# Kernel optimization log

Measured on AMD Instinct MI355X. Metric: run time of the kernel, lower is better.

The kernel has to match this reference:

```python
import jax, jax.numpy as jnp
import numpy as np
import math

N_HEADS = 16
D_HEAD = 128
D_ROPE = 32
SPLIT = D_HEAD - D_ROPE  # 96
LATENT = 512
D_MODEL = 2048
B, T = 2, 2048


def _rotary_emb(num_tokens, d_rope):
    inv_freq = 1.0 / (10000.0 ** (jnp.arange(0, d_rope, 2, dtype=jnp.float32) / d_rope))
    t = jnp.arange(num_tokens, dtype=jnp.float32)
    freqs = jnp.einsum('t,f->tf', t, inv_freq)          # [T, d_rope/2]
    return jnp.concatenate([freqs, freqs], axis=-1)      # [T, d_rope]


def _apply_rotary(x, cos, sin):
    # x: [B,T,H,d_rope]; cos/sin: [1,T,1,d_rope]
    half = x.shape[-1] // 2
    x1, x2 = x[..., :half], x[..., half:]
    rot = jnp.concatenate([-x2, x1], axis=-1)
    return x * cos + rot * sin


def setup_inputs() -> dict:
    key = jax.random.key(0)
    ks = jax.random.split(key, 20)
    s = 0.02
    def w(k, i, o):
        return jax.random.normal(k, (i, o), dtype=jnp.float32) * s
    inp = {
        'input': jax.random.normal(ks[0], (B, T, D_MODEL), dtype=jnp.float32),
        'batch_size': B,
        'num_tokens': T,
        'Wdkv_w': w(ks[1], D_MODEL, LATENT), 'Wdkv_b': jnp.zeros((LATENT,), jnp.float32),
        'Wdq_w':  w(ks[2], D_MODEL, LATENT), 'Wdq_b':  jnp.zeros((LATENT,), jnp.float32),
        'Wuk_w':  w(ks[3], LATENT, N_HEADS * SPLIT),  'Wuk_b': jnp.zeros((N_HEADS * SPLIT,), jnp.float32),
        'Wuv_w':  w(ks[4], LATENT, N_HEADS * D_HEAD), 'Wuv_b': jnp.zeros((N_HEADS * D_HEAD,), jnp.float32),
        'Wuq_w':  w(ks[5], LATENT, N_HEADS * SPLIT),  'Wuq_b': jnp.zeros((N_HEADS * SPLIT,), jnp.float32),
        'Wqr_w':  w(ks[6], LATENT, N_HEADS * D_ROPE), 'Wqr_b': jnp.zeros((N_HEADS * D_ROPE,), jnp.float32),
        'Wkr_w':  w(ks[7], D_MODEL, N_HEADS * D_ROPE), 'Wkr_b': jnp.zeros((N_HEADS * D_ROPE,), jnp.float32),
        'Wo_w':   w(ks[8], N_HEADS * D_HEAD, D_MODEL), 'Wo_b': jnp.zeros((D_MODEL,), jnp.float32),
    }
    return inp


def reference(input, batch_size, num_tokens,
              Wdkv_w, Wdkv_b, Wdq_w, Wdq_b, Wuk_w, Wuk_b, Wuv_w, Wuv_b,
              Wuq_w, Wuq_b, Wqr_w, Wqr_b, Wkr_w, Wkr_b, Wo_w, Wo_b):
    lin = lambda x, w, b: x @ w + b
    bsz, T_ = batch_size, num_tokens

    c_kv = lin(input, Wdkv_w, Wdkv_b)                                   # [B,T,latent]
    k_base = lin(c_kv, Wuk_w, Wuk_b).reshape(bsz, T_, N_HEADS, SPLIT)
    v = lin(c_kv, Wuv_w, Wuv_b).reshape(bsz, T_, N_HEADS, D_HEAD)

    c_q = lin(input, Wdq_w, Wdq_b)
    q_base = lin(c_q, Wuq_w, Wuq_b).reshape(bsz, T_, N_HEADS, SPLIT)
    q_rot = lin(c_q, Wqr_w, Wqr_b).reshape(bsz, T_, N_HEADS, D_ROPE)

    emb = _rotary_emb(T_, D_ROPE)                                        # [T,d_rope]
    cos = jnp.cos(emb)[None, :, None, :]
    sin = jnp.sin(emb)[None, :, None, :]
    q_rot = _apply_rotary(q_rot, cos, sin)
    k_rot = _apply_rotary(lin(input, Wkr_w, Wkr_b).reshape(bsz, T_, N_HEADS, D_ROPE), cos, sin)

    q = jnp.concatenate([q_base, q_rot], axis=-1)                        # [B,T,H,d_head]
    k = jnp.concatenate([k_base, k_rot], axis=-1)

    scores = jnp.einsum('bqhd,bkhd->bhqk', q, k) / math.sqrt(D_HEAD)
    attn = jax.nn.softmax(scores, axis=-1)
    out = jnp.einsum('bhqk,bkhd->bqhd', attn, v)
    out = lin(out.reshape(bsz, T_, N_HEADS * D_HEAD), Wo_w, Wo_b)
    return out, c_kv, k_rot
```

## Files before the change

### kernel.cpp

```cpp
#include <hip/hip_runtime.h>

typedef __bf16 bf16x8 __attribute__((ext_vector_type(8)));
typedef float f32x4 __attribute__((ext_vector_type(4)));
typedef float f32x16 __attribute__((ext_vector_type(16)));

#define NROWS 4096
#define DM 2048
#define LAT 512
#define NH 16
#define DH 128

__device__ __forceinline__ unsigned short f2bf(float f) {
    union { float f; unsigned u; } v; v.f = f;
    unsigned r = v.u + 0x7fffu + ((v.u >> 16) & 1u);
    return (unsigned short)(r >> 16);
}
__device__ __forceinline__ void gload16(const void* g, void* l) {
    __builtin_amdgcn_global_load_lds((const __attribute__((address_space(1))) unsigned int*)g,
                                     (__attribute__((address_space(3))) unsigned int*)l, 16, 0, 0);
}
__device__ __forceinline__ unsigned cvtpk_bf16(float lo, float hi) {
    unsigned r;
    asm("v_cvt_pk_bf16_f32 %0, %1, %2" : "=v"(r) : "v"(lo), "v"(hi));
    return r;
}
__device__ __forceinline__ void pl32swap(unsigned& a, unsigned& b) {
    asm("v_permlane32_swap_b32 %0, %1" : "+v"(a), "+v"(b));
}
__device__ __forceinline__ float exp2a(float x) {
    float r;
    asm("v_exp_f32 %0, %1" : "=v"(r) : "v"(x));
    return r;
}

struct PrepParams {
    const float* tsrc[8]; unsigned short* tdst[8];
    int tK[8]; int tN[8]; int tstart[8];
    const float* input; unsigned short* xbf;
    float* cs; float* sn;
    const float* bsrc[8]; float* bdst[8]; int blen[8];
};

#define PREP_T_END   9984
#define PREP_X_END   18176
#define PREP_R_END   18304
#define PREP_B_END   18340

__global__ __launch_bounds__(256) void prep_kernel(PrepParams P) {
    const int bid = blockIdx.x, tid = threadIdx.x;
    if (bid < PREP_T_END) {
        int j = 0;
        #pragma unroll
        for (int i = 1; i < 8; ++i) if (bid >= P.tstart[i]) j = i;
        const int local = bid - P.tstart[j];
        const float* W = P.tsrc[j];
        unsigned short* Wt = P.tdst[j];
        const int K = P.tK[j], N = P.tN[j];
        const int nbx = N >> 5;
        const int nb = (local % nbx) * 32, kb = (local / nbx) * 32;
        __shared__ float tile[32][33];
        const int tx = tid & 31, ty = tid >> 5;
        #pragma unroll
        for (int i = 0; i < 32; i += 8)
            tile[ty + i][tx] = W[(size_t)(kb + ty + i) * N + nb + tx];
        __syncthreads();
        #pragma unroll
        for (int i = 0; i < 32; i += 8)
            Wt[(size_t)(nb + ty + i) * K + kb + tx] = f2bf(tile[tx][ty + i]);
    } else if (bid < PREP_X_END) {
        const int i = ((bid - PREP_T_END) * 256 + tid) * 4;
        float4 v = *(const float4*)(P.input + i);
        unsigned short* y = P.xbf + i;
        y[0] = f2bf(v.x); y[1] = f2bf(v.y); y[2] = f2bf(v.z); y[3] = f2bf(v.w);
    } else if (bid < PREP_R_END) {
        const int idx = (bid - PREP_X_END) * 256 + tid;
        const int i = idx & 15, t = idx >> 4;
        float inv = powf(10000.0f, -(float)i / 16.0f);
        float a = (float)t * inv;
        P.cs[idx] = cosf(a);
        P.sn[idx] = sinf(a);
    } else {
        const int gid = (bid - PREP_R_END) * 256 + tid;
        int off = 0;
        #pragma unroll
        for (int i = 0; i < 8; ++i) {
            if (gid >= off && gid < off + P.blen[i])
                P.bdst[i][gid - off] = P.bsrc[i][gid - off];
            off += P.blen[i];
        }
    }
}

__global__ __launch_bounds__(256) void gemm_fused_kernel(const unsigned short* __restrict__ A,
                                                         const unsigned short* __restrict__ Bt,
                                                         const float* __restrict__ biascat,
                                                         int K, int which,
                                                         float* __restrict__ outF,
                                                         unsigned short* __restrict__ outB0,
                                                         unsigned short* __restrict__ outB1,
                                                         unsigned short* __restrict__ outB0k,
                                                         float* __restrict__ outRope,
                                                         const float* __restrict__ cs,
                                                         const float* __restrict__ sn) {
    __shared__ __align__(16) unsigned short SM[9216];
    unsigned short* As = SM;
    unsigned short* Bs = SM + 4096;
    const int tid = threadIdx.x;
    const int mb = blockIdx.x * 128;
    const int by = blockIdx.y, nb = by * 128;
    const int w = tid >> 6, lane = tid & 63;
    const int wr = (w >> 1) * 64, wc = (w & 1) * 64;
    const int l15 = lane & 15, l4 = lane >> 4;
    const int srow = lane >> 2, sko = (lane & 3) * 8;

    f32x4 acc[4][4] = {};

    for (int k0 = 0; k0 < K; k0 += 32) {
        __syncthreads();
        #pragma unroll
        for (int c = 0; c < 16; c += 4) {
            int cc = c + w;
            if (cc < 8)
                gload16(A + (size_t)(mb + cc * 16 + srow) * K + k0 + sko, As + cc * 512);
            else
                gload16(Bt + (size_t)(nb + (cc - 8) * 16 + srow) * K + k0 + sko, Bs + (cc - 8) * 512);
        }
        __syncthreads();
        bf16x8 af[4], bfr[4];
        #pragma unroll
        for (int mi = 0; mi < 4; ++mi)
            af[mi] = *(const bf16x8*)(As + (wr + mi * 16 + l15) * 32 + l4 * 8);
        #pragma unroll
        for (int ni = 0; ni < 4; ++ni)
            bfr[ni] = *(const bf16x8*)(Bs + (wc + ni * 16 + l15) * 32 + l4 * 8);
        #pragma unroll
        for (int mi = 0; mi < 4; ++mi)
            #pragma unroll
            for (int ni = 0; ni < 4; ++ni)
                acc[mi][ni] = __builtin_amdgcn_mfma_f32_16x16x32_bf16(af[mi], bfr[ni], acc[mi][ni], 0, 0, 0);
    }

    if (which == 1 && by >= 12) {
        const int c2b = nb - 1536;
        #pragma unroll
        for (int half = 0; half < 2; ++half) {
            __syncthreads();
            if ((wr >> 6) == half) {
                #pragma unroll
                for (int mi = 0; mi < 4; ++mi)
                    #pragma unroll
                    for (int ni = 0; ni < 4; ++ni) {
                        const int col = wc + ni * 16 + l15;
                        const float bv = biascat[nb + col];
                        ushort4 pv;
                        pv.x = f2bf(acc[mi][ni][0] + bv);
                        pv.y = f2bf(acc[mi][ni][1] + bv);
                        pv.z = f2bf(acc[mi][ni][2] + bv);
                        pv.w = f2bf(acc[mi][ni][3] + bv);
                        *(ushort4*)(SM + col * 72 + mi * 16 + l4 * 4) = pv;
                    }
            }
            __syncthreads();
            const int c = tid >> 1;
            #pragma unroll
            for (int j = 0; j < 4; ++j) {
                const int seg = (tid & 1) * 4 + j;
                uint4 val = *(const uint4*)(SM + c * 72 + seg * 8);
                *(uint4*)(outB1 + (size_t)(c2b + c) * 4096 + mb + half * 64 + seg * 8) = val;
            }
        }
        return;
    }

    #pragma unroll
    for (int mi = 0; mi < 4; ++mi) {
        const int row0 = mb + wr + mi * 16 + l4 * 4;
        #pragma unroll
        for (int ni = 0; ni < 4; ++ni) {
            const int colg = nb + wc + ni * 16 + l15;
            const float bv = biascat[colg];
            float v[4];
            #pragma unroll
            for (int r = 0; r < 4; ++r) v[r] = acc[mi][ni][r] + bv;

            if (which == 0) {
                if (by < 4) {
                    #pragma unroll
                    for (int r = 0; r < 4; ++r) {
                        outF[(size_t)(row0 + r) * 512 + colg] = v[r];
                        outB0[(size_t)(row0 + r) * 512 + colg] = f2bf(v[r]);
                    }
                } else if (by < 8) {
                    const int c2 = colg - 512;
                    #pragma unroll
                    for (int r = 0; r < 4; ++r)
                        outB1[(size_t)(row0 + r) * 512 + c2] = f2bf(v[r]);
                } else {
                    const int cloc = colg - 1024, i2 = cloc & 31, h2 = cloc >> 5;
                    const float pbv = biascat[colg ^ 16];
                    const bool lo = (ni & 1) == 0;
                    #pragma unroll
                    for (int r = 0; r < 4; ++r) {
                        float vp = acc[mi][ni ^ 1][r] + pbv;
                        int t = (row0 + r) & 2047;
                        float cc_ = cs[t * 16 + (i2 & 15)], ss_ = sn[t * 16 + (i2 & 15)];
                        float o = lo ? (v[r] * cc_ - vp * ss_) : (v[r] * cc_ + vp * ss_);
                        outRope[(size_t)(row0 + r) * 512 + cloc] = o;
                        outB0k[(size_t)(row0 + r) * 2048 + h2 * 128 + 96 + i2] = f2bf(o);
                    }
                }
            } else if (which == 1) {
                const int ocol = (colg / 96) * 128 + colg % 96;
                #pragma unroll
                for (int r = 0; r < 4; ++r)
                    outB0[(size_t)(row0 + r) * 2048 + ocol] = f2bf(v[r]);
            } else if (which == 2) {
                if (by < 12) {
                    const int ocol = (colg / 96) * 128 + colg % 96;
                    #pragma unroll
                    for (int r = 0; r < 4; ++r)
                        outB0[(size_t)(row0 + r) * 2048 + ocol] = f2bf(v[r]);
                } else {
                    const int cloc = colg - 1536, i2 = cloc & 31, h2 = cloc >> 5;
                    const float pbv = biascat[colg ^ 16];
                    const bool lo = (ni & 1) == 0;
                    #pragma unroll
                    for (int r = 0; r < 4; ++r) {
                        float vp = acc[mi][ni ^ 1][r] + pbv;
                        int t = (row0 + r) & 2047;
                        float cc_ = cs[t * 16 + (i2 & 15)], ss_ = sn[t * 16 + (i2 & 15)];
                        float o = lo ? (v[r] * cc_ - vp * ss_) : (v[r] * cc_ + vp * ss_);
                        outB0[(size_t)(row0 + r) * 2048 + h2 * 128 + 96 + i2] = f2bf(o);
                    }
                }
            } else {
                #pragma unroll
                for (int r = 0; r < 4; ++r)
                    outF[(size_t)(row0 + r) * 2048 + colg] = v[r];
            }
        }
    }
}

__global__ __launch_bounds__(256, 2) void attn_kernel(const unsigned short* __restrict__ Q,
                                                      const unsigned short* __restrict__ Kb,
                                                      const unsigned short* __restrict__ Vtg,
                                                      unsigned short* __restrict__ O) {
    __shared__ __align__(16) unsigned short Ks[2][64 * 128];
    __shared__ __align__(16) unsigned short Vs[2][128 * 64];

    const int tid = threadIdx.x, w = tid >> 6, lane = tid & 63;
    const int l31 = lane & 31, hi = lane >> 5;
    const int bh = blockIdx.y, b = bh >> 4, h = bh & 15;
    const int qrow = blockIdx.x * 128 + w * 32 + l31;
    const float sl2e = 0.08838834764831845f * 1.4426950408889634f;

    bf16x8 qf[8];
    const unsigned short* qptr = Q + (size_t)(b * 2048 + qrow) * 2048 + h * 128 + hi * 8;
    #pragma unroll
    for (int s = 0; s < 8; ++s) qf[s] = *(const bf16x8*)(qptr + s * 16);

    f32x16 acc[4] = {};
    float m_run = -1e30f, l_run = 0.0f;

    const int kl15 = lane >> 4, kd0 = lane & 15;
    const int vr = lane >> 3, vk = lane & 7;

    auto STAGE = [&](int buf, int kt) {
        #pragma unroll
        for (int i = 0; i < 4; ++i) {
            int c = w * 4 + i;
            int key = c * 4 + kl15;
            int d0 = (kd0 * 8) ^ ((key & 7) << 3);
            gload16(Kb + (size_t)(b * 2048 + kt + key) * 2048 + h * 128 + d0, &Ks[buf][c * 512]);
            int dv = c * 8 + vr;
            int k0 = (vk * 8) ^ ((dv & 7) << 3);
            gload16(Vtg + (size_t)(h * 128 + dv) * 4096 + b * 2048 + kt + k0, &Vs[buf][c * 512]);
        }
    };

    STAGE(0, 0);
    __syncthreads();

    for (int t = 0; t < 32; ++t) {
        const int buf = t & 1;
        if (t < 31) STAGE(buf ^ 1, (t + 1) * 64);

        #pragma unroll
        for (int g = 0; g < 2; ++g) {
            const int key = g * 32 + l31;
            const unsigned short* kbase = &Ks[buf][key * 128];
            const int ksw = (key & 7) << 3;
            f32x16 sc = {};
            __builtin_amdgcn_s_setprio(1);
            #pragma unroll
            for (int s = 0; s < 8; ++s) {
                bf16x8 kf = *(const bf16x8*)(kbase + ((s * 16 + hi * 8) ^ ksw));
                sc = __builtin_amdgcn_mfma_f32_32x32x16_bf16(kf, qf[s], sc, 0, 0, 0);
            }
            __builtin_amdgcn_s_setprio(0);

            float pm = sc[0];
            #pragma unroll
            for (int i = 1; i < 16; ++i) pm = fmaxf(pm, sc[i]);
            pm = fmaxf(pm, __shfl_xor(pm, 32, 64));

            if (__any(pm > m_run + 90.51f)) {
                float mn = fmaxf(m_run, pm);
                float f = exp2a((m_run - mn) * sl2e);
                m_run = mn;
                l_run *= f;
                #pragma unroll
                for (int dg = 0; dg < 4; ++dg)
                    #pragma unroll
                    for (int i = 0; i < 16; ++i) acc[dg][i] *= f;
            }
            const float mexp2 = m_run * sl2e;

            float rs = 0.0f;
            #pragma unroll
            for (int s2 = 0; s2 < 2; ++s2) {
                float e[8];
                #pragma unroll
                for (int j = 0; j < 8; ++j) {
                    e[j] = exp2a(fmaf(sc[s2 * 8 + j], sl2e, -mexp2));
                    rs += e[j];
                }
                unsigned X0 = cvtpk_bf16(e[0], e[1]), X1 = cvtpk_bf16(e[2], e[3]);
                unsigned Y0 = cvtpk_bf16(e[4], e[5]), Y1 = cvtpk_bf16(e[6], e[7]);
                pl32swap(X0, Y0);
                pl32swap(X1, Y1);
                union { unsigned u[4]; bf16x8 v; } pf;
                pf.u[0] = X0; pf.u[1] = X1; pf.u[2] = Y0; pf.u[3] = Y1;

                const int kofs = g * 32 + s2 * 16 + hi * 8;
                __builtin_amdgcn_s_setprio(1);
                #pragma unroll
                for (int dg = 0; dg < 4; ++dg) {
                    const int d = dg * 32 + l31;
                    bf16x8 vf = *(const bf16x8*)(&Vs[buf][d * 64 + (kofs ^ ((d & 7) << 3))]);
                    acc[dg] = __builtin_amdgcn_mfma_f32_32x32x16_bf16(vf, pf.v, acc[dg], 0, 0, 0);
                }
                __builtin_amdgcn_s_setprio(0);
            }
            rs += __shfl_xor(rs, 32, 64);
            l_run += rs;
        }
        __syncthreads();
    }

    const float inv = 1.0f / l_run;
    unsigned short* obase = O + (size_t)(b * 2048 + qrow) * 2048 + h * 128;
    #pragma unroll
    for (int dg = 0; dg < 4; ++dg)
        #pragma unroll
        for (int k = 0; k < 4; ++k) {
            ushort4 pv;
            pv.x = f2bf(acc[dg][4 * k + 0] * inv);
            pv.y = f2bf(acc[dg][4 * k + 1] * inv);
            pv.z = f2bf(acc[dg][4 * k + 2] * inv);
            pv.w = f2bf(acc[dg][4 * k + 3] * inv);
            *(ushort4*)(obase + dg * 32 + k * 8 + hi * 4) = pv;
        }
}

extern "C" void kernel_launch(void* const* d_in, const int* in_sizes, int n_in,
                              void* d_out, int out_size, void* d_ws, size_t ws_size,
                              hipStream_t stream) {
    (void)in_sizes; (void)n_in; (void)out_size; (void)ws_size;

    const float* input  = (const float*)d_in[0];
    const float* Wdkv_w = (const float*)d_in[3];
    const float* Wdkv_b = (const float*)d_in[4];
    const float* Wdq_w  = (const float*)d_in[5];
    const float* Wdq_b  = (const float*)d_in[6];
    const float* Wuk_w  = (const float*)d_in[7];
    const float* Wuk_b  = (const float*)d_in[8];
    const float* Wuv_w  = (const float*)d_in[9];
    const float* Wuv_b  = (const float*)d_in[10];
    const float* Wuq_w  = (const float*)d_in[11];
    const float* Wuq_b  = (const float*)d_in[12];
    const float* Wqr_w  = (const float*)d_in[13];
    const float* Wqr_b  = (const float*)d_in[14];
    const float* Wkr_w  = (const float*)d_in[15];
    const float* Wkr_b  = (const float*)d_in[16];
    const float* Wo_w   = (const float*)d_in[17];
    const float* Wo_b   = (const float*)d_in[18];

    float* out_main = (float*)d_out;
    float* out_ckv  = out_main + (size_t)NROWS * DM;
    float* out_krot = out_ckv + (size_t)NROWS * LAT;

    char* p = (char*)d_ws;
    auto alloc = [&](size_t bytes) { char* r = p; p += (bytes + 255) & ~(size_t)255; return r; };
    unsigned short* x_bf  = (unsigned short*)alloc((size_t)NROWS * DM * 2);
    unsigned short* w1_t  = (unsigned short*)alloc((size_t)1536 * DM * 2);
    unsigned short* w2_t  = (unsigned short*)alloc((size_t)3584 * LAT * 2);
    unsigned short* w3_t  = (unsigned short*)alloc((size_t)2048 * LAT * 2);
    unsigned short* w4_t  = (unsigned short*)alloc((size_t)DM * DM * 2);
    unsigned short* ckv_bf = (unsigned short*)alloc((size_t)NROWS * LAT * 2);
    unsigned short* cq_bf  = (unsigned short*)alloc((size_t)NROWS * LAT * 2);
    unsigned short* q_bf   = (unsigned short*)alloc((size_t)NROWS * DM * 2);
    unsigned short* k_bf   = (unsigned short*)alloc((size_t)NROWS * DM * 2);
    unsigned short* vt_g   = (unsigned short*)alloc((size_t)DM * NROWS * 2);
    unsigned short* ao_bf  = (unsigned short*)alloc((size_t)NROWS * DM * 2);
    float* cos_t = (float*)alloc((size_t)2048 * 16 * 4);
    float* sin_t = (float*)alloc((size_t)2048 * 16 * 4);
    float* bc1 = (float*)alloc(1536 * 4);
    float* bc2 = (float*)alloc(3584 * 4);
    float* bc3 = (float*)alloc(2048 * 4);
    float* bc4 = (float*)alloc(2048 * 4);

    PrepParams P;
    const float* tsrc[8] = {Wdkv_w, Wdq_w, Wkr_w, Wuk_w, Wuv_w, Wuq_w, Wqr_w, Wo_w};
    unsigned short* tdst[8] = {w1_t, w1_t + 512 * 2048, w1_t + 1024 * 2048,
                               w2_t, w2_t + 1536 * 512, w3_t, w3_t + 1536 * 512, w4_t};
    int tK[8] = {2048, 2048, 2048, 512, 512, 512, 512, 2048};
    int tN[8] = {512, 512, 512, 1536, 2048, 1536, 512, 2048};
    int tstart[8] = {0, 1024, 2048, 3072, 3840, 4864, 5632, 5888};
    const float* bsrc[8] = {Wdkv_b, Wdq_b, Wkr_b, Wuk_b, Wuv_b, Wuq_b, Wqr_b, Wo_b};
    float* bdst[8] = {bc1, bc1 + 512, bc1 + 1024, bc2, bc2 + 1536, bc3, bc3 + 1536, bc4};
    int blen[8] = {512, 512, 512, 1536, 2048, 1536, 512, 2048};
    for (int i = 0; i < 8; ++i) {
        P.tsrc[i] = tsrc[i]; P.tdst[i] = tdst[i]; P.tK[i] = tK[i]; P.tN[i] = tN[i];
        P.tstart[i] = tstart[i]; P.bsrc[i] = bsrc[i]; P.bdst[i] = bdst[i]; P.blen[i] = blen[i];
    }
    P.input = input; P.xbf = x_bf; P.cs = cos_t; P.sn = sin_t;
    prep_kernel<<<PREP_B_END, 256, 0, stream>>>(P);

    gemm_fused_kernel<<<dim3(32, 12), 256, 0, stream>>>(x_bf, w1_t, bc1, 2048, 0,
                                                        out_ckv, ckv_bf, cq_bf, k_bf, out_krot, cos_t, sin_t);
    gemm_fused_kernel<<<dim3(32, 28), 256, 0, stream>>>(ckv_bf, w2_t, bc2, 512, 1,
                                                        nullptr, k_bf, vt_g, nullptr, nullptr, nullptr, nullptr);
    gemm_fused_kernel<<<dim3(32, 16), 256, 0, stream>>>(cq_bf, w3_t, bc3, 512, 2,
                                                        nullptr, q_bf, nullptr, nullptr, nullptr, cos_t, sin_t);

    attn_kernel<<<dim3(16, 2 * NH), 256, 0, stream>>>(q_bf, k_bf, vt_g, ao_bf);

    gemm_fused_kernel<<<dim3(32, 16), 256, 0, stream>>>(ao_bf, w4_t, bc4, 2048, 3,
                                                        out_main, nullptr, nullptr, nullptr, nullptr, nullptr, nullptr);
}
```

Measured before the change: 259.0 us.

## Double-buffer GEMM LDS tiles, use fine-grained vmcnt waits, remap attention blocks across XCDs

The GEMM main loop now double-buffers its A/B tiles in LDS, prefetching the next K-slice while MFMAs run on the current one, with explicit vmcnt waits and raw barriers in place of two full __syncthreads per iteration. The attention kernel replaces __syncthreads with a partial vmcnt wait plus s_barrier, so the next K/V tile's loads stay in flight. Attention launches as a 1D grid whose block index is remapped so consecutive blocks spread across the 8 XCDs while blocks sharing a head share an XCD's L2. This doubles GEMM LDS use, which may lower occupancy, and relies on hand-counted vmcnt values being correct.

```diff
diff --git a/kernel.cpp b/kernel.cpp
--- a/kernel.cpp
+++ b/kernel.cpp
@@ -102,9 +102,7 @@
                                                          float* __restrict__ outRope,
                                                          const float* __restrict__ cs,
                                                          const float* __restrict__ sn) {
-    __shared__ __align__(16) unsigned short SM[9216];
-    unsigned short* As = SM;
-    unsigned short* Bs = SM + 4096;
+    __shared__ __align__(16) unsigned short SM[2][8192];
     const int tid = threadIdx.x;
     const int mb = blockIdx.x * 128;
     const int by = blockIdx.y, nb = by * 128;
@@ -115,17 +113,33 @@
 
     f32x4 acc[4][4] = {};
 
-    for (int k0 = 0; k0 < K; k0 += 32) {
-        __syncthreads();
+    auto STAGE = [&](int buf, int k0) {
         #pragma unroll
         for (int c = 0; c < 16; c += 4) {
             int cc = c + w;
             if (cc < 8)
-                gload16(A + (size_t)(mb + cc * 16 + srow) * K + k0 + sko, As + cc * 512);
+                gload16(A + (size_t)(mb + cc * 16 + srow) * K + k0 + sko, SM[buf] + cc * 512);
             else
-                gload16(Bt + (size_t)(nb + (cc - 8) * 16 + srow) * K + k0 + sko, Bs + (cc - 8) * 512);
-        }
-        __syncthreads();
+                gload16(Bt + (size_t)(nb + (cc - 8) * 16 + srow) * K + k0 + sko, SM[buf] + 4096 + (cc - 8) * 512);
+        }
+    };
+
+    const int nk = K >> 5;
+    STAGE(0, 0);
+    for (int kt = 0; kt < nk; ++kt) {
+        const int buf = kt & 1;
+        if (kt + 1 < nk) {
+            STAGE(buf ^ 1, (kt + 1) << 5);
+            asm volatile("s_waitcnt vmcnt(4)" ::: "memory");
+        } else {
+            asm volatile("s_waitcnt vmcnt(0)" ::: "memory");
+        }
+        __builtin_amdgcn_sched_barrier(0);
+        __builtin_amdgcn_s_barrier();
+        __builtin_amdgcn_sched_barrier(0);
+
+        const unsigned short* As = SM[buf];
+        const unsigned short* Bs = SM[buf] + 4096;
         bf16x8 af[4], bfr[4];
         #pragma unroll
         for (int mi = 0; mi < 4; ++mi)
@@ -138,9 +152,11 @@
             #pragma unroll
             for (int ni = 0; ni < 4; ++ni)
                 acc[mi][ni] = __builtin_amdgcn_mfma_f32_16x16x32_bf16(af[mi], bfr[ni], acc[mi][ni], 0, 0, 0);
+        __builtin_amdgcn_s_barrier();
     }
 
     if (which == 1 && by >= 12) {
+        unsigned short* BT = &SM[0][0];
         const int c2b = nb - 1536;
         #pragma unroll
         for (int half = 0; half < 2; ++half) {
@@ -157,7 +173,7 @@
                         pv.y = f2bf(acc[mi][ni][1] + bv);
                         pv.z = f2bf(acc[mi][ni][2] + bv);
                         pv.w = f2bf(acc[mi][ni][3] + bv);
-                        *(ushort4*)(SM + col * 72 + mi * 16 + l4 * 4) = pv;
+                        *(ushort4*)(BT + col * 72 + mi * 16 + l4 * 4) = pv;
                     }
             }
             __syncthreads();
@@ -165,7 +181,7 @@
             #pragma unroll
             for (int j = 0; j < 4; ++j) {
                 const int seg = (tid & 1) * 4 + j;
-                uint4 val = *(const uint4*)(SM + c * 72 + seg * 8);
+                uint4 val = *(const uint4*)(BT + c * 72 + seg * 8);
                 *(uint4*)(outB1 + (size_t)(c2b + c) * 4096 + mb + half * 64 + seg * 8) = val;
             }
         }
@@ -251,8 +267,11 @@
 
     const int tid = threadIdx.x, w = tid >> 6, lane = tid & 63;
     const int l31 = lane & 31, hi = lane >> 5;
-    const int bh = blockIdx.y, b = bh >> 4, h = bh & 15;
-    const int qrow = blockIdx.x * 128 + w * 32 + l31;
+    const int bid = blockIdx.x;
+    const int logical = (bid & 7) * 64 + (bid >> 3);
+    const int bh = logical >> 4, b = bh >> 4, h = bh & 15;
+    const int qt = (logical & 15) * 128 + w * 32;
+    const int qrow = qt + l31;
     const float sl2e = 0.08838834764831845f * 1.4426950408889634f;
 
     bf16x8 qf[8];
@@ -280,11 +299,18 @@
     };
 
     STAGE(0, 0);
-    __syncthreads();
 
     for (int t = 0; t < 32; ++t) {
         const int buf = t & 1;
-        if (t < 31) STAGE(buf ^ 1, (t + 1) * 64);
+        if (t < 31) {
+            STAGE(buf ^ 1, (t + 1) * 64);
+            asm volatile("s_waitcnt vmcnt(8)" ::: "memory");
+        } else {
+            asm volatile("s_waitcnt vmcnt(0)" ::: "memory");
+        }
+        __builtin_amdgcn_sched_barrier(0);
+        __builtin_amdgcn_s_barrier();
+        __builtin_amdgcn_sched_barrier(0);
 
         #pragma unroll
         for (int g = 0; g < 2; ++g) {
@@ -346,7 +372,7 @@
             rs += __shfl_xor(rs, 32, 64);
             l_run += rs;
         }
-        __syncthreads();
+        __builtin_amdgcn_s_barrier();
     }
 
     const float inv = 1.0f / l_run;
@@ -435,7 +461,7 @@
     gemm_fused_kernel<<<dim3(32, 16), 256, 0, stream>>>(cq_bf, w3_t, bc3, 512, 2,
                                                         nullptr, q_bf, nullptr, nullptr, nullptr, cos_t, sin_t);
 
-    attn_kernel<<<dim3(16, 2 * NH), 256, 0, stream>>>(q_bf, k_bf, vt_g, ao_bf);
+    attn_kernel<<<512, 256, 0, stream>>>(q_bf, k_bf, vt_g, ao_bf);
 
     gemm_fused_kernel<<<dim3(32, 16), 256, 0, stream>>>(ao_bf, w4_t, bc4, 2048, 3,
                                                         out_main, nullptr, nullptr, nullptr, nullptr, nullptr, nullptr);
```

Result: faster. 239.0 us (-7.7%).
